# Optimization experiments

Measured on AMD Instinct MI355X. Metric: run time of the kernel, lower is better.

The kernel has to match this reference:

```python
import jax, jax.numpy as jnp
import numpy as np

B, N, F_IN, HID, OUT = 4096, 116, 116, 256, 2


def setup_inputs() -> dict:
    key = jax.random.key(0)
    ks = jax.random.split(key, 10)
    x = jax.random.normal(ks[0], (B, N, F_IN), dtype=jnp.float32)
    support = jax.random.uniform(ks[1], (B, N, N), dtype=jnp.float32) / N  # row-normalized-ish adjacency
    s = 0.05
    W1 = jax.random.normal(ks[2], (F_IN, HID), dtype=jnp.float32) * s
    b1 = jnp.zeros((HID,), dtype=jnp.float32)
    W2 = jax.random.normal(ks[3], (HID, OUT * 2), dtype=jnp.float32) * s
    b2 = jnp.zeros((OUT * 2,), dtype=jnp.float32)
    Wr1 = jax.random.normal(ks[4], (N * OUT * 2, 64), dtype=jnp.float32) * s
    br1 = jnp.zeros((64,), dtype=jnp.float32)
    Wr2 = jax.random.normal(ks[5], (64, OUT), dtype=jnp.float32) * s
    br2 = jnp.zeros((OUT,), dtype=jnp.float32)
    return {"x": x, "support": support, "W1": W1, "b1": b1, "W2": W2,
            "b2": b2, "Wr1": Wr1, "br1": br1, "Wr2": Wr2, "br2": br2}


def graph_conv(x, support, W, b):
    # GraphConv: activation(support @ (x @ W) + b)
    xw = jnp.einsum('bnf,fh->bnh', x, W)
    h = jnp.einsum('bnm,bmh->bnh', support, xw) + b
    return jax.nn.relu(h)


def reference(x, support, W1, b1, W2, b2, Wr1, br1, Wr2, br2):
    h = graph_conv(x, support, W1, b1)          # [B, N, HID]
    h = graph_conv(h, support, W2, b2)          # [B, N, 2*OUT]
    flat = h.reshape(h.shape[0], -1)            # [B, N*2*OUT]
    r = jax.nn.relu(flat @ Wr1 + br1)           # [B, 64]
    logits = r @ Wr2 + br2                      # [B, OUT]
    return jax.nn.log_softmax(logits, axis=-1)
```

## Files before the change

kernel.cpp:

```cpp
#include <hip/hip_runtime.h>
#include <math.h>


#define BDIM 512

constexpr int Bsz = 4096;
constexpr int Nn  = 116;
constexpr int Fin = 116;
constexpr int HID = 256;
constexpr int SK  = 136;
constexpr int NF4 = 3364;
constexpr int W1T_ELEMS = 256 * SK;
constexpr int W2T_OFF   = W1T_ELEMS;

typedef __bf16 bf16;
typedef __bf16 bf16x4 __attribute__((ext_vector_type(4)));
typedef __bf16 bf16x8 __attribute__((ext_vector_type(8)));
typedef float  floatx4 __attribute__((ext_vector_type(4)));


__global__ __launch_bounds__(1024) void prep_weights(
    const float* __restrict__ W1, const float* __restrict__ W2,
    bf16* __restrict__ WT)
{
  int j = blockIdx.x * 1024 + threadIdx.x;
  if (j < W1T_ELEMS) {
    int h = j / SK, kk = j - h * SK;
    WT[j] = (bf16)((kk < Fin) ? W1[kk * HID + h] : 0.f);
  } else if (j < W1T_ELEMS + 4 * 264) {
    int t = j - W1T_ELEMS;
    int n = t / 264, k = t - n * 264;
    WT[j] = (bf16)((k < HID) ? W2[k * 4 + n] : 0.f);
  }
}

__global__ __launch_bounds__(BDIM, 2) void gcn_fused(
    const float* __restrict__ X, const float* __restrict__ SUPP,
    const bf16* __restrict__ WT,
    const float* __restrict__ B1v, const float* __restrict__ B2v,
    const float* __restrict__ Wr1, const float* __restrict__ br1,
    const float* __restrict__ Wr2, const float* __restrict__ br2,
    float* __restrict__ OUTP)
{
  __shared__ __align__(16) bf16 sx  [128 * SK];
  __shared__ __align__(16) bf16 ssup[128 * SK];
  __shared__ __align__(16) bf16 swb [128 * SK];
  __shared__ __align__(16) bf16 sh1c[128 * SK];
  __shared__ __align__(16) bf16 sw2t[4 * 264];
  __shared__ __align__(16) bf16 stt [4 * SK];
  __shared__ float sh2[464];
  __shared__ float spart[8 * 64];

  const int b    = blockIdx.x;
  const int tid  = threadIdx.x;
  const int wid  = tid >> 6;
  const int lane = tid & 63;
  const int quad = lane >> 4;
  const int l16  = lane & 15;

  const float4* xg = (const float4*)(X    + (size_t)b * (Nn * Fin));
  const float4* sg = (const float4*)(SUPP + (size_t)b * (Nn * Fin));
  for (int i = tid; i < NF4; i += BDIM) {
    int m  = i / 29;
    int kq = (i - m * 29) * 4;
    float4 v = xg[i];
    bf16x4 p; p[0]=(bf16)v.x; p[1]=(bf16)v.y; p[2]=(bf16)v.z; p[3]=(bf16)v.w;
    *(bf16x4*)&sx[m * SK + kq] = p;
    float4 u = sg[i];
    bf16x4 q; q[0]=(bf16)u.x; q[1]=(bf16)u.y; q[2]=(bf16)u.z; q[3]=(bf16)u.w;
    *(bf16x4*)&ssup[m * SK + kq] = q;
  }
  for (int i = tid; i < 128 * 5; i += BDIM) {
    int m = i / 5, cc = 116 + (i - m * 5) * 4;
    bf16x4 z; z[0]=z[1]=z[2]=z[3]=(bf16)0.f;
    *(bf16x4*)&sx[m * SK + cc] = z;
    *(bf16x4*)&ssup[m * SK + cc] = z;
  }
  {
    const float4* wsrc = (const float4*)WT;
    float4* wdst = (float4*)swb;
    for (int i = tid; i < 2176; i += BDIM) wdst[i] = wsrc[i];
    const float4* w2src = (const float4*)(WT + W2T_OFF);
    if (tid < 132) ((float4*)sw2t)[tid] = w2src[tid];
  }

  const int wm = (wid & 1) * 64;
  const int wn = (wid >> 1) * 32;

  floatx4 acc3; acc3[0]=acc3[1]=acc3[2]=acc3[3]=0.f;

  for (int c = 0; c < 2; ++c) {
    if (c == 1) {
      const float4* wsrc = (const float4*)(WT + 128 * SK);
      float4* wdst = (float4*)swb;
      for (int i = tid; i < 2176; i += BDIM) wdst[i] = wsrc[i];
#pragma unroll
      for (int ks = 0; ks < 4; ++ks) {
        int k0 = ks * 32 + quad * 8;
        bf16x8 bfr = *(const bf16x8*)&sw2t[(l16 & 3) * 264 + k0];
        bf16x8 af  = *(const bf16x8*)&sh1c[(wid * 16 + l16) * SK + k0];
        acc3 = __builtin_amdgcn_mfma_f32_16x16x32_bf16(af, bfr, acc3, 0, 0, 0);
      }
    }
    __syncthreads();

    floatx4 acc[4][2];
#pragma unroll
    for (int mt = 0; mt < 4; ++mt)
#pragma unroll
      for (int nt = 0; nt < 2; ++nt) { acc[mt][nt][0]=acc[mt][nt][1]=acc[mt][nt][2]=acc[mt][nt][3]=0.f; }
#pragma unroll
    for (int ks = 0; ks < 4; ++ks) {
      int k0 = ks * 32 + quad * 8;
      bf16x8 af[4], bfr[2];
#pragma unroll
      for (int mt = 0; mt < 4; ++mt)
        af[mt] = *(const bf16x8*)&sx[(wm + mt * 16 + l16) * SK + k0];
#pragma unroll
      for (int nt = 0; nt < 2; ++nt)
        bfr[nt] = *(const bf16x8*)&swb[(wn + nt * 16 + l16) * SK + k0];
#pragma unroll
      for (int mt = 0; mt < 4; ++mt)
#pragma unroll
        for (int nt = 0; nt < 2; ++nt)
          acc[mt][nt] = __builtin_amdgcn_mfma_f32_16x16x32_bf16(af[mt], bfr[nt], acc[mt][nt], 0, 0, 0);
    }
    __syncthreads();

#pragma unroll
    for (int mt = 0; mt < 4; ++mt)
#pragma unroll
      for (int nt = 0; nt < 2; ++nt) {
        int mb = wm + mt * 16 + quad * 4;
        int n  = wn + nt * 16 + l16;
        floatx4 a = acc[mt][nt];
        bf16x4 p;
        if (mb < Nn) { p[0]=(bf16)a[0]; p[1]=(bf16)a[1]; p[2]=(bf16)a[2]; p[3]=(bf16)a[3]; }
        else         { p[0]=p[1]=p[2]=p[3]=(bf16)0.f; }
        *(bf16x4*)&swb[n * SK + mb] = p;
      }
    __syncthreads();

#pragma unroll
    for (int mt = 0; mt < 4; ++mt)
#pragma unroll
      for (int nt = 0; nt < 2; ++nt) { acc[mt][nt][0]=acc[mt][nt][1]=acc[mt][nt][2]=acc[mt][nt][3]=0.f; }
#pragma unroll
    for (int ks = 0; ks < 4; ++ks) {
      int k0 = ks * 32 + quad * 8;
      bf16x8 af[4], bfr[2];
#pragma unroll
      for (int mt = 0; mt < 4; ++mt)
        af[mt] = *(const bf16x8*)&ssup[(wm + mt * 16 + l16) * SK + k0];
#pragma unroll
      for (int nt = 0; nt < 2; ++nt)
        bfr[nt] = *(const bf16x8*)&swb[(wn + nt * 16 + l16) * SK + k0];
#pragma unroll
      for (int mt = 0; mt < 4; ++mt)
#pragma unroll
        for (int nt = 0; nt < 2; ++nt)
          acc[mt][nt] = __builtin_amdgcn_mfma_f32_16x16x32_bf16(af[mt], bfr[nt], acc[mt][nt], 0, 0, 0);
    }
#pragma unroll
    for (int mt = 0; mt < 4; ++mt)
#pragma unroll
      for (int nt = 0; nt < 2; ++nt) {
        int mb   = wm + mt * 16 + quad * 4;
        int coll = wn + nt * 16 + l16;
        float bb = B1v[c * 128 + coll];
        floatx4 a = acc[mt][nt];
#pragma unroll
        for (int r = 0; r < 4; ++r)
          sh1c[(mb + r) * SK + coll] = (bf16)fmaxf(a[r] + bb, 0.f);
      }
    __syncthreads();
  }

#pragma unroll
  for (int ks = 0; ks < 4; ++ks) {
    int k0 = ks * 32 + quad * 8;
    bf16x8 bfr = *(const bf16x8*)&sw2t[(l16 & 3) * 264 + 128 + k0];
    bf16x8 af  = *(const bf16x8*)&sh1c[(wid * 16 + l16) * SK + k0];
    acc3 = __builtin_amdgcn_mfma_f32_16x16x32_bf16(af, bfr, acc3, 0, 0, 0);
  }
  {
    int mb = wid * 16 + quad * 4;
    bf16x4 p;
    if (mb < Nn) { p[0]=(bf16)acc3[0]; p[1]=(bf16)acc3[1]; p[2]=(bf16)acc3[2]; p[3]=(bf16)acc3[3]; }
    else         { p[0]=p[1]=p[2]=p[3]=(bf16)0.f; }
    if (l16 < 4) *(bf16x4*)&stt[l16 * SK + mb] = p;
  }
  __syncthreads();

  floatx4 acc4; acc4[0]=acc4[1]=acc4[2]=acc4[3]=0.f;
#pragma unroll
  for (int ks = 0; ks < 4; ++ks) {
    int k0 = ks * 32 + quad * 8;
    bf16x8 af  = *(const bf16x8*)&ssup[(wid * 16 + l16) * SK + k0];
    bf16x8 bfr = *(const bf16x8*)&stt[(l16 & 3) * SK + k0];
    acc4 = __builtin_amdgcn_mfma_f32_16x16x32_bf16(af, bfr, acc4, 0, 0, 0);
  }
  if (l16 < 4) {
    float bb = B2v[l16];
#pragma unroll
    for (int r = 0; r < 4; ++r) {
      int m = wid * 16 + quad * 4 + r;
      if (m < Nn) sh2[m * 4 + l16] = fmaxf(acc4[r] + bb, 0.f);
    }
  }
  __syncthreads();

  {
    int j   = tid & 63;
    int ksl = tid >> 6;
    int kb  = ksl * 58;
    float p = 0.f;
#pragma unroll 2
    for (int kk = 0; kk < 58; ++kk)
      p = fmaf(sh2[kb + kk], Wr1[(kb + kk) * 64 + j], p);
    spart[ksl * 64 + j] = p;
  }
  __syncthreads();
  if (tid < 64) {
    int j = tid;
    float r = 0.f;
#pragma unroll
    for (int s = 0; s < 8; ++s) r += spart[s * 64 + j];
    r = fmaxf(r + br1[j], 0.f);
    float p0 = r * Wr2[j * 2 + 0];
    float p1 = r * Wr2[j * 2 + 1];
#pragma unroll
    for (int off = 32; off > 0; off >>= 1) {
      p0 += __shfl_xor(p0, off, 64);
      p1 += __shfl_xor(p1, off, 64);
    }
    float l0 = p0 + br2[0], l1 = p1 + br2[1];
    float mx  = fmaxf(l0, l1);
    float lse = mx + logf(expf(l0 - mx) + expf(l1 - mx));
    if (j < 2) OUTP[(size_t)b * 2 + j] = (j ? l1 : l0) - lse;
  }
}

extern "C" void kernel_launch(void* const* d_in, const int* in_sizes, int n_in,
                              void* d_out, int out_size, void* d_ws, size_t ws_size,
                              hipStream_t stream) {
  const float* X    = (const float*)d_in[0];
  const float* SUPP = (const float*)d_in[1];
  const float* W1   = (const float*)d_in[2];
  const float* B1v  = (const float*)d_in[3];
  const float* W2   = (const float*)d_in[4];
  const float* B2v  = (const float*)d_in[5];
  const float* Wr1  = (const float*)d_in[6];
  const float* br1  = (const float*)d_in[7];
  const float* Wr2  = (const float*)d_in[8];
  const float* br2  = (const float*)d_in[9];
  bf16* WT = (bf16*)d_ws;

  prep_weights<<<36, 1024, 0, stream>>>(W1, W2, WT);
  gcn_fused<<<Bsz, BDIM, 0, stream>>>(X, SUPP, WT, B1v, B2v,
                                      Wr1, br1, Wr2, br2, (float*)d_out);
}
```

Baseline: 648.2 us.

## Cut LDS footprint by streaming X from global and reusing weight buffer

Result: faster. 607.2 us (-6.3%).

```diff
diff --git a/kernel.cpp b/kernel.cpp
--- a/kernel.cpp
+++ b/kernel.cpp
@@ -34,7 +34,16 @@
   }
 }
 
-__global__ __launch_bounds__(BDIM, 2) void gcn_fused(
+__device__ inline bf16x8 cvt8(const float* p) {
+  float4 v0 = *(const float4*)p;
+  float4 v1 = *(const float4*)(p + 4);
+  bf16x8 f;
+  f[0]=(bf16)v0.x; f[1]=(bf16)v0.y; f[2]=(bf16)v0.z; f[3]=(bf16)v0.w;
+  f[4]=(bf16)v1.x; f[5]=(bf16)v1.y; f[6]=(bf16)v1.z; f[7]=(bf16)v1.w;
+  return f;
+}
+
+__global__ __launch_bounds__(BDIM, 4) void gcn_fused(
     const float* __restrict__ X, const float* __restrict__ SUPP,
     const bf16* __restrict__ WT,
     const float* __restrict__ B1v, const float* __restrict__ B2v,
@@ -42,10 +51,8 @@
     const float* __restrict__ Wr2, const float* __restrict__ br2,
     float* __restrict__ OUTP)
 {
-  __shared__ __align__(16) bf16 sx  [128 * SK];
   __shared__ __align__(16) bf16 ssup[128 * SK];
   __shared__ __align__(16) bf16 swb [128 * SK];
-  __shared__ __align__(16) bf16 sh1c[128 * SK];
   __shared__ __align__(16) bf16 sw2t[4 * 264];
   __shared__ __align__(16) bf16 stt [4 * SK];
   __shared__ float sh2[464];
@@ -58,79 +65,83 @@
   const int quad = lane >> 4;
   const int l16  = lane & 15;
 
-  const float4* xg = (const float4*)(X    + (size_t)b * (Nn * Fin));
+  const int wm = (wid & 3) * 32;
+  const int wn = (wid >> 2) * 64;
+
   const float4* sg = (const float4*)(SUPP + (size_t)b * (Nn * Fin));
   for (int i = tid; i < NF4; i += BDIM) {
     int m  = i / 29;
     int kq = (i - m * 29) * 4;
-    float4 v = xg[i];
-    bf16x4 p; p[0]=(bf16)v.x; p[1]=(bf16)v.y; p[2]=(bf16)v.z; p[3]=(bf16)v.w;
-    *(bf16x4*)&sx[m * SK + kq] = p;
     float4 u = sg[i];
     bf16x4 q; q[0]=(bf16)u.x; q[1]=(bf16)u.y; q[2]=(bf16)u.z; q[3]=(bf16)u.w;
     *(bf16x4*)&ssup[m * SK + kq] = q;
   }
-  for (int i = tid; i < 128 * 5; i += BDIM) {
-    int m = i / 5, cc = 116 + (i - m * 5) * 4;
+  {
     bf16x4 z; z[0]=z[1]=z[2]=z[3]=(bf16)0.f;
-    *(bf16x4*)&sx[m * SK + cc] = z;
-    *(bf16x4*)&ssup[m * SK + cc] = z;
-  }
-  {
-    const float4* wsrc = (const float4*)WT;
-    float4* wdst = (float4*)swb;
-    for (int i = tid; i < 2176; i += BDIM) wdst[i] = wsrc[i];
-    const float4* w2src = (const float4*)(WT + W2T_OFF);
-    if (tid < 132) ((float4*)sw2t)[tid] = w2src[tid];
-  }
-
-  const int wm = (wid & 1) * 64;
-  const int wn = (wid >> 1) * 32;
-
+    for (int i = tid; i < 128 * 5; i += BDIM) {
+      int m = i / 5, cc = 116 + (i - m * 5) * 4;
+      *(bf16x4*)&ssup[m * SK + cc] = z;
+    }
+    for (int i = tid; i < 12 * 29; i += BDIM) {
+      int r = 116 + i / 29, cc = (i - (i / 29) * 29) * 4;
+      *(bf16x4*)&ssup[r * SK + cc] = z;
+    }
+  }
+  for (int i = tid; i < 2176; i += BDIM)
+    ((float4*)swb)[i] = ((const float4*)WT)[i];
+  if (tid < 132) ((float4*)sw2t)[tid] = ((const float4*)(WT + W2T_OFF))[tid];
+  __syncthreads();
+
+  const float* xrow = X + (size_t)b * (Nn * Fin);
   floatx4 acc3; acc3[0]=acc3[1]=acc3[2]=acc3[3]=0.f;
 
   for (int c = 0; c < 2; ++c) {
     if (c == 1) {
-      const float4* wsrc = (const float4*)(WT + 128 * SK);
-      float4* wdst = (float4*)swb;
-      for (int i = tid; i < 2176; i += BDIM) wdst[i] = wsrc[i];
-#pragma unroll
-      for (int ks = 0; ks < 4; ++ks) {
-        int k0 = ks * 32 + quad * 8;
-        bf16x8 bfr = *(const bf16x8*)&sw2t[(l16 & 3) * 264 + k0];
-        bf16x8 af  = *(const bf16x8*)&sh1c[(wid * 16 + l16) * SK + k0];
-        acc3 = __builtin_amdgcn_mfma_f32_16x16x32_bf16(af, bfr, acc3, 0, 0, 0);
+      for (int i = tid; i < 2176; i += BDIM)
+        ((float4*)swb)[i] = ((const float4*)(WT + 128 * SK))[i];
+      __syncthreads();
+    }
+
+    floatx4 acc[2][4];
+#pragma unroll
+    for (int mt = 0; mt < 2; ++mt)
+#pragma unroll
+      for (int nt = 0; nt < 4; ++nt) { acc[mt][nt][0]=acc[mt][nt][1]=acc[mt][nt][2]=acc[mt][nt][3]=0.f; }
+#pragma unroll
+    for (int ks = 0; ks < 4; ++ks) {
+      const int k0 = ks * 32 + quad * 8;
+      bf16x8 af[2];
+#pragma unroll
+      for (int mt = 0; mt < 2; ++mt) {
+        int row  = wm + mt * 16 + l16;
+        int rowc = row < Nn ? row : (Nn - 1);
+        const float* p = xrow + rowc * Fin + k0;
+        if (ks < 3) {
+          af[mt] = cvt8(p);
+        } else {
+          bf16x8 f;
+#pragma unroll
+          for (int j = 0; j < 8; ++j)
+            f[j] = (k0 + j < Fin) ? (bf16)p[j] : (bf16)0.f;
+          af[mt] = f;
+        }
       }
-    }
-    __syncthreads();
-
-    floatx4 acc[4][2];
-#pragma unroll
-    for (int mt = 0; mt < 4; ++mt)
-#pragma unroll
-      for (int nt = 0; nt < 2; ++nt) { acc[mt][nt][0]=acc[mt][nt][1]=acc[mt][nt][2]=acc[mt][nt][3]=0.f; }
-#pragma unroll
-    for (int ks = 0; ks < 4; ++ks) {
-      int k0 = ks * 32 + quad * 8;
-      bf16x8 af[4], bfr[2];
-#pragma unroll
-      for (int mt = 0; mt < 4; ++mt)
-        af[mt] = *(const bf16x8*)&sx[(wm + mt * 16 + l16) * SK + k0];
-#pragma unroll
-      for (int nt = 0; nt < 2; ++nt)
+      bf16x8 bfr[4];
+#pragma unroll
+      for (int nt = 0; nt < 4; ++nt)
         bfr[nt] = *(const bf16x8*)&swb[(wn + nt * 16 + l16) * SK + k0];
 #pragma unroll
-      for (int mt = 0; mt < 4; ++mt)
-#pragma unroll
-        for (int nt = 0; nt < 2; ++nt)
+      for (int mt = 0; mt < 2; ++mt)
+#pragma unroll
+        for (int nt = 0; nt < 4; ++nt)
           acc[mt][nt] = __builtin_amdgcn_mfma_f32_16x16x32_bf16(af[mt], bfr[nt], acc[mt][nt], 0, 0, 0);
     }
     __syncthreads();
 
 #pragma unroll
-    for (int mt = 0; mt < 4; ++mt)
-#pragma unroll
-      for (int nt = 0; nt < 2; ++nt) {
+    for (int mt = 0; mt < 2; ++mt)
+#pragma unroll
+      for (int nt = 0; nt < 4; ++nt) {
         int mb = wm + mt * 16 + quad * 4;
         int n  = wn + nt * 16 + l16;
         floatx4 a = acc[mt][nt];
@@ -142,47 +153,51 @@
     __syncthreads();
 
 #pragma unroll
-    for (int mt = 0; mt < 4; ++mt)
-#pragma unroll
-      for (int nt = 0; nt < 2; ++nt) { acc[mt][nt][0]=acc[mt][nt][1]=acc[mt][nt][2]=acc[mt][nt][3]=0.f; }
+    for (int mt = 0; mt < 2; ++mt)
+#pragma unroll
+      for (int nt = 0; nt < 4; ++nt) { acc[mt][nt][0]=acc[mt][nt][1]=acc[mt][nt][2]=acc[mt][nt][3]=0.f; }
 #pragma unroll
     for (int ks = 0; ks < 4; ++ks) {
-      int k0 = ks * 32 + quad * 8;
-      bf16x8 af[4], bfr[2];
-#pragma unroll
-      for (int mt = 0; mt < 4; ++mt)
+      const int k0 = ks * 32 + quad * 8;
+      bf16x8 af[2], bfr[4];
+#pragma unroll
+      for (int mt = 0; mt < 2; ++mt)
         af[mt] = *(const bf16x8*)&ssup[(wm + mt * 16 + l16) * SK + k0];
 #pragma unroll
-      for (int nt = 0; nt < 2; ++nt)
+      for (int nt = 0; nt < 4; ++nt)
         bfr[nt] = *(const bf16x8*)&swb[(wn + nt * 16 + l16) * SK + k0];
 #pragma unroll
-      for (int mt = 0; mt < 4; ++mt)
-#pragma unroll
-        for (int nt = 0; nt < 2; ++nt)
+      for (int mt = 0; mt < 2; ++mt)
+#pragma unroll
+        for (int nt = 0; nt < 4; ++nt)
           acc[mt][nt] = __builtin_amdgcn_mfma_f32_16x16x32_bf16(af[mt], bfr[nt], acc[mt][nt], 0, 0, 0);
     }
-#pragma unroll
-    for (int mt = 0; mt < 4; ++mt)
-#pragma unroll
-      for (int nt = 0; nt < 2; ++nt) {
+    __syncthreads();
+
+#pragma unroll
+    for (int mt = 0; mt < 2; ++mt)
+#pragma unroll
+      for (int nt = 0; nt < 4; ++nt) {
         int mb   = wm + mt * 16 + quad * 4;
         int coll = wn + nt * 16 + l16;
         float bb = B1v[c * 128 + coll];
         floatx4 a = acc[mt][nt];
 #pragma unroll
         for (int r = 0; r < 4; ++r)
-          sh1c[(mb + r) * SK + coll] = (bf16)fmaxf(a[r] + bb, 0.f);
+          swb[(mb + r) * SK + coll] = (bf16)fmaxf(a[r] + bb, 0.f);
       }
     __syncthreads();
-  }
-
-#pragma unroll
-  for (int ks = 0; ks < 4; ++ks) {
-    int k0 = ks * 32 + quad * 8;
-    bf16x8 bfr = *(const bf16x8*)&sw2t[(l16 & 3) * 264 + 128 + k0];
-    bf16x8 af  = *(const bf16x8*)&sh1c[(wid * 16 + l16) * SK + k0];
-    acc3 = __builtin_amdgcn_mfma_f32_16x16x32_bf16(af, bfr, acc3, 0, 0, 0);
-  }
+
+#pragma unroll
+    for (int ks = 0; ks < 4; ++ks) {
+      const int k0 = ks * 32 + quad * 8;
+      bf16x8 bfr = *(const bf16x8*)&sw2t[(l16 & 3) * 264 + c * 128 + k0];
+      bf16x8 af  = *(const bf16x8*)&swb[(wid * 16 + l16) * SK + k0];
+      acc3 = __builtin_amdgcn_mfma_f32_16x16x32_bf16(af, bfr, acc3, 0, 0, 0);
+    }
+    if (c == 0) __syncthreads();
+  }
+
   {
     int mb = wid * 16 + quad * 4;
     bf16x4 p;
@@ -195,7 +210,7 @@
   floatx4 acc4; acc4[0]=acc4[1]=acc4[2]=acc4[3]=0.f;
 #pragma unroll
   for (int ks = 0; ks < 4; ++ks) {
-    int k0 = ks * 32 + quad * 8;
+    const int k0 = ks * 32 + quad * 8;
     bf16x8 af  = *(const bf16x8*)&ssup[(wid * 16 + l16) * SK + k0];
     bf16x8 bfr = *(const bf16x8*)&stt[(l16 & 3) * SK + k0];
     acc4 = __builtin_amdgcn_mfma_f32_16x16x32_bf16(af, bfr, acc4, 0, 0, 0);
```
